# Optimization experiments

Measured on AMD Instinct MI355X. Metric: run time of the kernel, lower is better.

## Reference

```python
import jax, jax.numpy as jnp
import numpy as np

EMBED = 2048
NUM_EXPERTS = 64
TOP_K = 8


def setup_inputs() -> dict:
    key = jax.random.key(0)
    k1, k2, k3 = jax.random.split(key, 3)
    inputs = jax.random.normal(k1, (8, 4096, EMBED), dtype=jnp.float32)
    # nn.Linear(embed_size, num_experts): weight [num_experts, embed_size], bias [num_experts]
    W = jax.random.normal(k2, (NUM_EXPERTS, EMBED), dtype=jnp.float32) / np.sqrt(EMBED)
    b = jax.random.normal(k3, (NUM_EXPERTS,), dtype=jnp.float32) * 0.01
    return {"inputs": inputs, "W": W, "b": b}


def reference(inputs, W, b):
    # Linear projection: [B, S, E] x [E, N] -> [B, S, N]
    logits = jnp.einsum('bse,ne->bsn', inputs, W) + b
    # top-k selection along expert axis
    _, indices = jax.lax.top_k(logits, TOP_K)  # [B, S, K] int32
    # scatter mask: 1 at selected experts (one_hot sum == scatter_ of ones)
    mask = jax.nn.one_hot(indices, NUM_EXPERTS, dtype=jnp.bool_).any(axis=-2)  # [B, S, N]
    # masked_fill(-inf) + softmax -> probs only on selected experts
    masked = jnp.where(mask, logits, -jnp.inf)
    probs = jax.nn.softmax(masked, axis=-1)
    return probs, indices
```

## Files before the change

kernel.cpp:

```cpp
#include <hip/hip_runtime.h>
#include <cmath>

#define NTOK 32768
#define EMB  2048
#define NEXP 64
#define TOPK 8
#define BT   128
#define KC   32
#define NCH  (EMB / KC)
#define TAU  1e-4f

typedef __attribute__((ext_vector_type(8))) short bf16x8;
typedef __attribute__((ext_vector_type(4))) float f32x4;

union U4 { unsigned int u[4]; bf16x8 v; };

__device__ __forceinline__ float uf(unsigned int x) { return __uint_as_float(x); }
__device__ __forceinline__ unsigned int fu(float x) { return __float_as_uint(x); }

__device__ __forceinline__ void gld16(const float* g, float* lds) {
    __builtin_amdgcn_global_load_lds(
        (const __attribute__((address_space(1))) void*)g,
        (__attribute__((address_space(3))) void*)lds,
        16, 0, 0);
}

__global__ __launch_bounds__(512, 2) void router_bf16x3(
    const float* __restrict__ X,
    const float* __restrict__ W,
    const float* __restrict__ Bv,
    float* __restrict__ out)
{
    __shared__ __align__(16) unsigned char smem[57344];
    float* xsBase          = (float*)smem;
    unsigned short* wsBase = (unsigned short*)(smem + 32768);
    float* lg              = (float*)smem;

    const int tid  = threadIdx.x;
    const int lane = tid & 63;
    const int w    = tid >> 6;
    const int tg   = w >> 1;
    const int eh   = w & 1;
    const int eL   = lane & 15;
    const int q    = lane >> 4;
    const int t0   = blockIdx.x * BT;

    f32x4 am[4], ac[4];
    #pragma unroll
    for (int t = 0; t < 4; ++t) {
        am[t] = (f32x4){0.f, 0.f, 0.f, 0.f};
        ac[t] = (f32x4){0.f, 0.f, 0.f, 0.f};
    }

    auto stageX = [&](int ch, int buf) {
        const int kc0 = ch * KC;
        float* dst = xsBase + buf * 4096;
        #pragma unroll
        for (int s = 0; s < 2; ++s) {
            const int instr = w * 2 + s;
            const int row   = instr * 8 + (lane >> 3);
            const int g     = (lane & 7) ^ (lane >> 3);
            gld16(&X[(size_t)(t0 + row) * EMB + kc0 + 4 * g], dst + instr * 256);
        }
    };

    auto loadW = [&](int ch) -> float4 {
        const int er = tid >> 3;
        const int h  = tid & 7;
        return *(const float4*)&W[(size_t)er * EMB + ch * KC + 4 * h];
    };
    auto putW = [&](float4 v, int buf) {
        const int er = tid >> 3, h = tid & 7, slot = h >> 1, sub = h & 1;
        unsigned short* base = wsBase + buf * 6144;
        unsigned int u0 = fu(v.x), u1 = fu(v.y), u2 = fu(v.z), u3 = fu(v.w);
        unsigned int p1a = (u0 >> 16) | (u1 & 0xffff0000u);
        unsigned int p1b = (u2 >> 16) | (u3 & 0xffff0000u);
        float r0 = v.x - uf(u0 & 0xffff0000u), r1 = v.y - uf(u1 & 0xffff0000u);
        float r2 = v.z - uf(u2 & 0xffff0000u), r3 = v.w - uf(u3 & 0xffff0000u);
        unsigned int w0 = fu(r0), w1 = fu(r1), w2 = fu(r2), w3 = fu(r3);
        unsigned int p2a = (w0 >> 16) | (w1 & 0xffff0000u);
        unsigned int p2b = (w2 >> 16) | (w3 & 0xffff0000u);
        float s0 = r0 - uf(w0 & 0xffff0000u), s1 = r1 - uf(w1 & 0xffff0000u);
        float s2 = r2 - uf(w2 & 0xffff0000u), s3 = r3 - uf(w3 & 0xffff0000u);
        unsigned int p3a = (fu(s0) >> 16) | (fu(s1) & 0xffff0000u);
        unsigned int p3b = (fu(s2) >> 16) | (fu(s3) & 0xffff0000u);
        const int off = slot * 512 + er * 8 + sub * 4;
        *(uint2*)(void*)(base + off)          = make_uint2(p1a, p1b);
        *(uint2*)(void*)(base + 2048 + off)   = make_uint2(p2a, p2b);
        *(uint2*)(void*)(base + 4096 + off)   = make_uint2(p3a, p3b);
    };

    auto compute = [&](int buf) {
        const float* xb          = xsBase + buf * 4096;
        const unsigned short* wb = wsBase + buf * 6144;
        bf16x8 Bf[2][3];
        #pragma unroll
        for (int cc = 0; cc < 2; ++cc) {
            const int er = eh * 32 + cc * 16 + eL;
            #pragma unroll
            for (int p = 0; p < 3; ++p)
                Bf[cc][p] = *(const bf16x8*)(const void*)(wb + p * 2048 + q * 512 + er * 8);
        }
        #pragma unroll
        for (int tt = 0; tt < 2; ++tt) {
            const int row = tg * 32 + tt * 16 + eL;
            const int sl  = (2 * q) ^ (eL & 7);
            const float4 aL = *(const float4*)&xb[row * 32 + 4 * sl];
            const float4 aH = *(const float4*)&xb[row * 32 + 4 * (sl ^ 1)];
            U4 A1, A2, A3;
            const float e0[8] = {aL.x, aL.y, aL.z, aL.w, aH.x, aH.y, aH.z, aH.w};
            #pragma unroll
            for (int m = 0; m < 4; ++m) {
                float x0 = e0[2*m], x1 = e0[2*m+1];
                unsigned int u0 = fu(x0), u1 = fu(x1);
                A1.u[m] = (u0 >> 16) | (u1 & 0xffff0000u);
                float r0 = x0 - uf(u0 & 0xffff0000u), r1 = x1 - uf(u1 & 0xffff0000u);
                unsigned int w0 = fu(r0), w1 = fu(r1);
                A2.u[m] = (w0 >> 16) | (w1 & 0xffff0000u);
                float s0 = r0 - uf(w0 & 0xffff0000u), s1 = r1 - uf(w1 & 0xffff0000u);
                A3.u[m] = (fu(s0) >> 16) | (fu(s1) & 0xffff0000u);
            }
            #pragma unroll
            for (int cc = 0; cc < 2; ++cc) {
                const int t = tt * 2 + cc;
                am[t] = __builtin_amdgcn_mfma_f32_16x16x32_bf16(A1.v, Bf[cc][0], am[t], 0,0,0);
                ac[t] = __builtin_amdgcn_mfma_f32_16x16x32_bf16(A1.v, Bf[cc][1], ac[t], 0,0,0);
                ac[t] = __builtin_amdgcn_mfma_f32_16x16x32_bf16(A2.v, Bf[cc][0], ac[t], 0,0,0);
                ac[t] = __builtin_amdgcn_mfma_f32_16x16x32_bf16(A1.v, Bf[cc][2], ac[t], 0,0,0);
                ac[t] = __builtin_amdgcn_mfma_f32_16x16x32_bf16(A2.v, Bf[cc][1], ac[t], 0,0,0);
                ac[t] = __builtin_amdgcn_mfma_f32_16x16x32_bf16(A3.v, Bf[cc][0], ac[t], 0,0,0);
            }
        }
    };

    stageX(0, 0);
    putW(loadW(0), 0);
    __syncthreads();
    for (int ch = 0; ch < NCH; ++ch) {
        const int cur = ch & 1;
        const bool pf = (ch + 1 < NCH);
        float4 nw;
        if (pf) { stageX(ch + 1, cur ^ 1); nw = loadW(ch + 1); }
        compute(cur);
        if (pf) putW(nw, cur ^ 1);
        __syncthreads();
    }

    float* probs = out;
    float* idxo  = out + (size_t)NTOK * NEXP;
    const float bb0 = Bv[eh * 32 + eL];
    const float bb1 = Bv[eh * 32 + 16 + eL];
    #pragma unroll
    for (int tt = 0; tt < 2; ++tt)
        #pragma unroll
        for (int cc = 0; cc < 2; ++cc) {
            const int t = tt * 2 + cc;
            const int e = eh * 32 + cc * 16 + eL;
            const float bbv = cc ? bb1 : bb0;
            #pragma unroll
            for (int i = 0; i < 4; ++i) {
                const int r = tg * 32 + tt * 16 + q * 4 + i;
                lg[r * 66 + e] = (am[t][i] + ac[t][i]) + bbv;
            }
        }
    __syncthreads();

    auto slowToken = [&](int Tg) {
        const float* xr = X + (size_t)Tg * EMB;
        const float* wr = W + (size_t)lane * EMB;
        double ex = (double)Bv[lane];
        for (int k = 0; k < EMB; k += 4) {
            const float4 xv = *(const float4*)&xr[k];
            const float4 wv = *(const float4*)&wr[k];
            ex += (double)xv.x * (double)wv.x;
            ex += (double)xv.y * (double)wv.y;
            ex += (double)xv.z * (double)wv.z;
            ex += (double)xv.w * (double)wv.w;
        }
        bool selb = false; int myrank = 0;
        double m0d = 0.0; float ss = 0.f;
        #pragma unroll
        for (int it = 0; it < TOPK; ++it) {
            double bv = selb ? -1.0e300 : ex; int be = lane;
            #pragma unroll
            for (int off = 1; off <= 32; off <<= 1) {
                const double ov = __shfl_xor(bv, off, 64);
                const int    oe = __shfl_xor(be, off, 64);
                if (ov > bv || (ov == bv && oe < be)) { bv = ov; be = oe; }
            }
            if (it == 0) m0d = bv;
            ss += __expf((float)(bv - m0d));
            if (lane == be) { selb = true; myrank = it; }
        }
        probs[(size_t)Tg * NEXP + lane] = selb ? __expf((float)(ex - m0d)) / ss : 0.f;
        if (selb) idxo[(size_t)Tg * TOPK + myrank] = (float)lane;
    };

    #pragma unroll
    for (int i = 0; i < 4; ++i) {
        const int T = w * 16 + q * 4 + i;
        float v[4];
        #pragma unroll
        for (int c = 0; c < 4; ++c) v[c] = lg[T * 66 + c * 16 + eL];

        unsigned sel = 0;
        float m0 = 0.f, ssum = 0.f, prev = 0.f, mingap = 1e30f;
        int myIdx = 0;
        #pragma unroll
        for (int it = 0; it <= TOPK; ++it) {
            float bv = -1e30f; int be = 1 << 30;
            #pragma unroll
            for (int c = 0; c < 4; ++c)
                if (!((sel >> c) & 1) && v[c] > bv) { bv = v[c]; be = c * 16 + eL; }
            float gv = bv; int ge = be;
            #pragma unroll
            for (int off = 1; off <= 8; off <<= 1) {
                const float ov = __shfl_xor(gv, off, 64);
                const int   oe = __shfl_xor(ge, off, 64);
                if (ov > gv || (ov == gv && oe < ge)) { gv = ov; ge = oe; }
            }
            if (it == 0) m0 = gv;
            else mingap = fminf(mingap, prev - gv);
            prev = gv;
            if (it < TOPK) {
                ssum += __expf(gv - m0);
                if ((ge & 15) == eL) sel |= 1u << (ge >> 4);
                if (eL == it) myIdx = ge;
            }
        }
        const int Tg = t0 + T;
        const float inv = 1.0f / ssum;
        #pragma unroll
        for (int c = 0; c < 4; ++c) {
            const float p = ((sel >> c) & 1) ? __expf(v[c] - m0) * inv : 0.0f;
            probs[(size_t)Tg * NEXP + c * 16 + eL] = p;
        }
        if (eL < TOPK) idxo[(size_t)Tg * TOPK + eL] = (float)myIdx;

        const unsigned long long fb = __ballot(mingap < TAU);
        for (int q2 = 0; q2 < 4; ++q2)
            if ((fb >> (q2 * 16)) & 1) slowToken(t0 + w * 16 + q2 * 4 + i);
    }
}

extern "C" void kernel_launch(void* const* d_in, const int* in_sizes, int n_in,
                              void* d_out, int out_size, void* d_ws, size_t ws_size,
                              hipStream_t stream) {
    const float* X = (const float*)d_in[0];
    const float* W = (const float*)d_in[1];
    const float* B = (const float*)d_in[2];
    router_bf16x3<<<NTOK / BT, 512, 0, stream>>>(X, W, B, (float*)d_out);
}
```

Measured before the change: 508.1 us.

## Halve token tile to 64 rows and unroll fp64 fallback dot product

```diff
diff --git a/kernel.cpp b/kernel.cpp
--- a/kernel.cpp
+++ b/kernel.cpp
@@ -5,7 +5,7 @@
 #define EMB  2048
 #define NEXP 64
 #define TOPK 8
-#define BT   128
+#define BT   64
 #define KC   32
 #define NCH  (EMB / KC)
 #define TAU  1e-4f
@@ -31,9 +31,9 @@
     const float* __restrict__ Bv,
     float* __restrict__ out)
 {
-    __shared__ __align__(16) unsigned char smem[57344];
+    __shared__ __align__(16) unsigned char smem[40960];
     float* xsBase          = (float*)smem;
-    unsigned short* wsBase = (unsigned short*)(smem + 32768);
+    unsigned short* wsBase = (unsigned short*)(smem + 16384);
     float* lg              = (float*)smem;
 
     const int tid  = threadIdx.x;
@@ -45,23 +45,19 @@
     const int q    = lane >> 4;
     const int t0   = blockIdx.x * BT;
 
-    f32x4 am[4], ac[4];
+    f32x4 am[2], ac[2];
     #pragma unroll
-    for (int t = 0; t < 4; ++t) {
+    for (int t = 0; t < 2; ++t) {
         am[t] = (f32x4){0.f, 0.f, 0.f, 0.f};
         ac[t] = (f32x4){0.f, 0.f, 0.f, 0.f};
     }
 
     auto stageX = [&](int ch, int buf) {
         const int kc0 = ch * KC;
-        float* dst = xsBase + buf * 4096;
-        #pragma unroll
-        for (int s = 0; s < 2; ++s) {
-            const int instr = w * 2 + s;
-            const int row   = instr * 8 + (lane >> 3);
-            const int g     = (lane & 7) ^ (lane >> 3);
-            gld16(&X[(size_t)(t0 + row) * EMB + kc0 + 4 * g], dst + instr * 256);
-        }
+        float* dst = xsBase + buf * 2048;
+        const int row = w * 8 + (lane >> 3);
+        const int g   = (lane & 7) ^ (lane >> 3);
+        gld16(&X[(size_t)(t0 + row) * EMB + kc0 + 4 * g], dst + w * 256);
     };
 
     auto loadW = [&](int ch) -> float4 {
@@ -91,7 +87,7 @@
     };
 
     auto compute = [&](int buf) {
-        const float* xb          = xsBase + buf * 4096;
+        const float* xb          = xsBase + buf * 2048;
         const unsigned short* wb = wsBase + buf * 6144;
         bf16x8 Bf[2][3];
         #pragma unroll
@@ -101,35 +97,31 @@
             for (int p = 0; p < 3; ++p)
                 Bf[cc][p] = *(const bf16x8*)(const void*)(wb + p * 2048 + q * 512 + er * 8);
         }
-        #pragma unroll
-        for (int tt = 0; tt < 2; ++tt) {
-            const int row = tg * 32 + tt * 16 + eL;
-            const int sl  = (2 * q) ^ (eL & 7);
-            const float4 aL = *(const float4*)&xb[row * 32 + 4 * sl];
-            const float4 aH = *(const float4*)&xb[row * 32 + 4 * (sl ^ 1)];
-            U4 A1, A2, A3;
-            const float e0[8] = {aL.x, aL.y, aL.z, aL.w, aH.x, aH.y, aH.z, aH.w};
-            #pragma unroll
-            for (int m = 0; m < 4; ++m) {
-                float x0 = e0[2*m], x1 = e0[2*m+1];
-                unsigned int u0 = fu(x0), u1 = fu(x1);
-                A1.u[m] = (u0 >> 16) | (u1 & 0xffff0000u);
-                float r0 = x0 - uf(u0 & 0xffff0000u), r1 = x1 - uf(u1 & 0xffff0000u);
-                unsigned int w0 = fu(r0), w1 = fu(r1);
-                A2.u[m] = (w0 >> 16) | (w1 & 0xffff0000u);
-                float s0 = r0 - uf(w0 & 0xffff0000u), s1 = r1 - uf(w1 & 0xffff0000u);
-                A3.u[m] = (fu(s0) >> 16) | (fu(s1) & 0xffff0000u);
-            }
-            #pragma unroll
-            for (int cc = 0; cc < 2; ++cc) {
-                const int t = tt * 2 + cc;
-                am[t] = __builtin_amdgcn_mfma_f32_16x16x32_bf16(A1.v, Bf[cc][0], am[t], 0,0,0);
-                ac[t] = __builtin_amdgcn_mfma_f32_16x16x32_bf16(A1.v, Bf[cc][1], ac[t], 0,0,0);
-                ac[t] = __builtin_amdgcn_mfma_f32_16x16x32_bf16(A2.v, Bf[cc][0], ac[t], 0,0,0);
-                ac[t] = __builtin_amdgcn_mfma_f32_16x16x32_bf16(A1.v, Bf[cc][2], ac[t], 0,0,0);
-                ac[t] = __builtin_amdgcn_mfma_f32_16x16x32_bf16(A2.v, Bf[cc][1], ac[t], 0,0,0);
-                ac[t] = __builtin_amdgcn_mfma_f32_16x16x32_bf16(A3.v, Bf[cc][0], ac[t], 0,0,0);
-            }
+        const int row = tg * 16 + eL;
+        const int sl  = (2 * q) ^ (eL & 7);
+        const float4 aL = *(const float4*)&xb[row * 32 + 4 * sl];
+        const float4 aH = *(const float4*)&xb[row * 32 + 4 * (sl ^ 1)];
+        U4 A1, A2, A3;
+        const float e0[8] = {aL.x, aL.y, aL.z, aL.w, aH.x, aH.y, aH.z, aH.w};
+        #pragma unroll
+        for (int m = 0; m < 4; ++m) {
+            float x0 = e0[2*m], x1 = e0[2*m+1];
+            unsigned int u0 = fu(x0), u1 = fu(x1);
+            A1.u[m] = (u0 >> 16) | (u1 & 0xffff0000u);
+            float r0 = x0 - uf(u0 & 0xffff0000u), r1 = x1 - uf(u1 & 0xffff0000u);
+            unsigned int w0 = fu(r0), w1 = fu(r1);
+            A2.u[m] = (w0 >> 16) | (w1 & 0xffff0000u);
+            float s0 = r0 - uf(w0 & 0xffff0000u), s1 = r1 - uf(w1 & 0xffff0000u);
+            A3.u[m] = (fu(s0) >> 16) | (fu(s1) & 0xffff0000u);
+        }
+        #pragma unroll
+        for (int cc = 0; cc < 2; ++cc) {
+            am[cc] = __builtin_amdgcn_mfma_f32_16x16x32_bf16(A1.v, Bf[cc][0], am[cc], 0,0,0);
+            ac[cc] = __builtin_amdgcn_mfma_f32_16x16x32_bf16(A1.v, Bf[cc][1], ac[cc], 0,0,0);
+            ac[cc] = __builtin_amdgcn_mfma_f32_16x16x32_bf16(A2.v, Bf[cc][0], ac[cc], 0,0,0);
+            ac[cc] = __builtin_amdgcn_mfma_f32_16x16x32_bf16(A1.v, Bf[cc][2], ac[cc], 0,0,0);
+            ac[cc] = __builtin_amdgcn_mfma_f32_16x16x32_bf16(A2.v, Bf[cc][1], ac[cc], 0,0,0);
+            ac[cc] = __builtin_amdgcn_mfma_f32_16x16x32_bf16(A3.v, Bf[cc][0], ac[cc], 0,0,0);
         }
     };
 
@@ -151,32 +143,40 @@
     const float bb0 = Bv[eh * 32 + eL];
     const float bb1 = Bv[eh * 32 + 16 + eL];
     #pragma unroll
-    for (int tt = 0; tt < 2; ++tt)
-        #pragma unroll
-        for (int cc = 0; cc < 2; ++cc) {
-            const int t = tt * 2 + cc;
-            const int e = eh * 32 + cc * 16 + eL;
-            const float bbv = cc ? bb1 : bb0;
-            #pragma unroll
-            for (int i = 0; i < 4; ++i) {
-                const int r = tg * 32 + tt * 16 + q * 4 + i;
-                lg[r * 66 + e] = (am[t][i] + ac[t][i]) + bbv;
-            }
-        }
+    for (int cc = 0; cc < 2; ++cc) {
+        const int e = eh * 32 + cc * 16 + eL;
+        const float bbv = cc ? bb1 : bb0;
+        #pragma unroll
+        for (int i = 0; i < 4; ++i) {
+            const int r = tg * 16 + q * 4 + i;
+            lg[r * 66 + e] = (am[cc][i] + ac[cc][i]) + bbv;
+        }
+    }
     __syncthreads();
 
     auto slowToken = [&](int Tg) {
         const float* xr = X + (size_t)Tg * EMB;
         const float* wr = W + (size_t)lane * EMB;
-        double ex = (double)Bv[lane];
-        for (int k = 0; k < EMB; k += 4) {
-            const float4 xv = *(const float4*)&xr[k];
-            const float4 wv = *(const float4*)&wr[k];
-            ex += (double)xv.x * (double)wv.x;
-            ex += (double)xv.y * (double)wv.y;
-            ex += (double)xv.z * (double)wv.z;
-            ex += (double)xv.w * (double)wv.w;
-        }
+        double s0 = 0.0, s1 = 0.0, s2 = 0.0, s3 = 0.0;
+        for (int k = 0; k < EMB; k += 16) {
+            const float4 xa = *(const float4*)&xr[k];
+            const float4 xb = *(const float4*)&xr[k + 4];
+            const float4 xc = *(const float4*)&xr[k + 8];
+            const float4 xd = *(const float4*)&xr[k + 12];
+            const float4 wa = *(const float4*)&wr[k];
+            const float4 wb = *(const float4*)&wr[k + 4];
+            const float4 wc = *(const float4*)&wr[k + 8];
+            const float4 wd = *(const float4*)&wr[k + 12];
+            s0 += (double)xa.x * wa.x + (double)xa.y * wa.y
+                + (double)xa.z * wa.z + (double)xa.w * wa.w;
+            s1 += (double)xb.x * wb.x + (double)xb.y * wb.y
+                + (double)xb.z * wb.z + (double)xb.w * wb.w;
+            s2 += (double)xc.x * wc.x + (double)xc.y * wc.y
+                + (double)xc.z * wc.z + (double)xc.w * wc.w;
+            s3 += (double)xd.x * wd.x + (double)xd.y * wd.y
+                + (double)xd.z * wd.z + (double)xd.w * wd.w;
+        }
+        double ex = (double)Bv[lane] + ((s0 + s1) + (s2 + s3));
         bool selb = false; int myrank = 0;
         double m0d = 0.0; float ss = 0.f;
         #pragma unroll
@@ -197,8 +197,8 @@
     };
 
     #pragma unroll
-    for (int i = 0; i < 4; ++i) {
-        const int T = w * 16 + q * 4 + i;
+    for (int i = 0; i < 2; ++i) {
+        const int T = w * 8 + i * 4 + q;
         float v[4];
         #pragma unroll
         for (int c = 0; c < 4; ++c) v[c] = lg[T * 66 + c * 16 + eL];
@@ -239,7 +239,7 @@
 
         const unsigned long long fb = __ballot(mingap < TAU);
         for (int q2 = 0; q2 < 4; ++q2)
-            if ((fb >> (q2 * 16)) & 1) slowToken(t0 + w * 16 + q2 * 4 + i);
+            if ((fb >> (q2 * 16)) & 1) slowToken(t0 + w * 8 + i * 4 + q2);
     }
 }
 
```

Measured after the change: 484.9 us. -4.6%, faster.
